# Optimization experiments

Measured on AMD Instinct MI355X. Metric: run time of the kernel, lower is better.

Reference implementation:

```python
import jax, jax.numpy as jnp
import numpy as np

NOISE_DIM = 100
HIDDEN = 256
VOCAB = 200
N_PHASES = 13
SEQ_LEN = 20
BATCH = 16384


def setup_inputs() -> dict:
    key = jax.random.key(0)
    ks = jax.random.split(key, 8)
    s = 0.05
    return {
        "noise": jax.random.normal(ks[0], (BATCH, NOISE_DIM), jnp.float32),
        "W_proj": jax.random.normal(ks[1], (HIDDEN, NOISE_DIM), jnp.float32) * s,
        "b_proj": jnp.zeros((HIDDEN,), jnp.float32),
        "W_ih": jax.random.normal(ks[2], (4 * HIDDEN, HIDDEN), jnp.float32) * s,
        "W_hh": jax.random.normal(ks[3], (4 * HIDDEN, HIDDEN), jnp.float32) * s,
        "b_ih": jnp.zeros((4 * HIDDEN,), jnp.float32),
        "b_hh": jnp.zeros((4 * HIDDEN,), jnp.float32),
        "W_tech": jax.random.normal(ks[4], (VOCAB, HIDDEN), jnp.float32) * s,
        "b_tech": jnp.zeros((VOCAB,), jnp.float32),
        "W_phase": jax.random.normal(ks[5], (N_PHASES, HIDDEN), jnp.float32) * s,
        "b_phase": jnp.zeros((N_PHASES,), jnp.float32),
        "W_time": jax.random.normal(ks[6], (1, HIDDEN), jnp.float32) * s,
        "b_time": jnp.zeros((1,), jnp.float32),
    }


def reference(noise, W_proj, b_proj, W_ih, W_hh, b_ih, b_hh,
              W_tech, b_tech, W_phase, b_phase, W_time, b_time):
    # initial_projection: x0 = Linear(noise)  -> first LSTM input
    x0 = noise @ W_proj.T + b_proj                      # [B, H]
    B = noise.shape[0]
    h0 = jnp.zeros((B, HIDDEN), noise.dtype)
    c0 = jnp.zeros((B, HIDDEN), noise.dtype)

    def step(carry, _):
        x, h, c = carry
        # torch LSTM gate order: i, f, g, o
        gates = x @ W_ih.T + b_ih + h @ W_hh.T + b_hh   # [B, 4H]
        i, f, g, o = jnp.split(gates, 4, axis=-1)
        i = jax.nn.sigmoid(i)
        f = jax.nn.sigmoid(f)
        g = jnp.tanh(g)
        o = jax.nn.sigmoid(o)
        c_new = f * c + i * g
        h_new = o * jnp.tanh(c_new)
        tech = h_new @ W_tech.T + b_tech                # [B, VOCAB]
        phase = h_new @ W_phase.T + b_phase             # [B, 13]
        timing = jax.nn.relu(h_new @ W_time.T + b_time) # [B, 1]
        out = jnp.concatenate([tech, phase, timing], axis=-1)  # [B, 214]
        # next step's LSTM input is the previous LSTM output (h_new)
        return (h_new, h_new, c_new), out

    _, outs = jax.lax.scan(step, (x0, h0, c0), None, length=SEQ_LEN)
    # outs: [SEQ_LEN, B, VOCAB + 13 + 1] = per-step [technique_logits | phase_logits | timing]
    return outs
```

## Files before the change

### kernel.cpp

```cpp
#include <hip/hip_runtime.h>
#include <stdint.h>

#define HID 256
#define BATCH 16384
#define SEQ 20
#define OUTF 214
#define BM 64
#define NBLK (BATCH/BM)
#define ROWE 264

typedef __attribute__((ext_vector_type(8))) short short8;
typedef __attribute__((ext_vector_type(4))) float f32x4;

#define MFMA(a,b,c) __builtin_amdgcn_mfma_f32_16x16x32_bf16((a),(b),(c),0,0,0)
#define SBAR() asm volatile("s_waitcnt lgkmcnt(0)\n\ts_barrier" ::: "memory")

__device__ __forceinline__ unsigned short f2bf(float f) {
    unsigned int u = __builtin_bit_cast(unsigned int, f);
    u += 0x7FFFu + ((u >> 16) & 1u);
    return (unsigned short)(u >> 16);
}
__device__ __forceinline__ float sigm(float x)     { return __fdividef(1.0f, 1.0f + __expf(-x)); }
__device__ __forceinline__ float tanhfast(float x) { return 1.0f - __fdividef(2.0f, __expf(2.0f*x) + 1.0f); }

__global__ __launch_bounds__(256) void prep_kernel(
    const float* __restrict__ W_proj, const float* __restrict__ W_ih,
    const float* __restrict__ W_hh,  const float* __restrict__ b_ih,
    const float* __restrict__ b_hh,  const float* __restrict__ W_tech,
    const float* __restrict__ b_tech, const float* __restrict__ W_phase,
    const float* __restrict__ b_phase, const float* __restrict__ W_time,
    const float* __restrict__ b_time,
    unsigned short* __restrict__ Wc, unsigned short* __restrict__ Wi,
    unsigned short* __restrict__ Wo, unsigned short* __restrict__ Wp,
    float* __restrict__ b_comb, float* __restrict__ b_out)
{
    const int n = blockIdx.x;
    const int k = threadIdx.x;
    const int lane = (n & 15) | (((k >> 3) & 3) << 4);
    const int e  = k & 7;
    const int tn = n >> 4;
    {
        float wi = W_ih[n*HID + k], wh = W_hh[n*HID + k];
        int idx = ((tn*8 + (k>>5))*64 + lane)*8 + e;
        Wi[idx] = f2bf(wi);
        Wc[idx] = f2bf(wi + wh);
    }
    if (n < 224) {
        float v = 0.0f;
        if (n < 200)       v = W_tech[n*HID + k];
        else if (n < 213)  v = W_phase[(n-200)*HID + k];
        else if (n == 213) v = W_time[k];
        int idx = ((tn*8 + (k>>5))*64 + lane)*8 + e;
        Wo[idx] = f2bf(v);
    }
    if (n < 256 && k < 128) {
        float v = (k < 100) ? W_proj[n*100 + k] : 0.0f;
        int idx = ((tn*4 + (k>>5))*64 + lane)*8 + e;
        Wp[idx] = f2bf(v);
    }
    if (n < 4) b_comb[n*256 + k] = b_ih[n*256 + k] + b_hh[n*256 + k];
    if (n == 4 && k < 224) {
        float v = 0.0f;
        if (k < 200)       v = b_tech[k];
        else if (k < 213)  v = b_phase[k-200];
        else if (k == 213) v = b_time[0];
        b_out[k] = v;
    }
}

__global__ __launch_bounds__(512, 2) void lstm_kernel(
    const float* __restrict__ noise, const float* __restrict__ b_proj,
    const unsigned short* __restrict__ Wc, const unsigned short* __restrict__ Wi,
    const unsigned short* __restrict__ Wo_g, const unsigned short* __restrict__ Wp,
    const float* __restrict__ b_comb, const float* __restrict__ b_out,
    float* __restrict__ out)
{
    __shared__ __attribute__((aligned(16))) unsigned short hbuf[2][BM * ROWE];
    __shared__ __attribute__((aligned(16))) float out_lds[BM * OUTF];

    const int tid  = threadIdx.x;
    const int w    = tid >> 6;
    const int lane = tid & 63;
    const int lr   = lane & 15;
    const int lq   = lane >> 4;
    const int blk  = blockIdx.x;

    {
        const float* nsrc = noise + (size_t)blk * BM * 100;
        for (int i = tid; i < BM*100; i += 512) {
            int m = i / 100; int kk = i - m*100;
            hbuf[1][m*ROWE + kk] = f2bf(nsrc[i]);
        }
        for (int i = tid; i < BM*28; i += 512) {
            int m = i / 28; int kk = i - m*28;
            hbuf[1][m*ROWE + 100 + kk] = 0;
        }
    }

    f32x4 bi[2][4];
    #pragma unroll
    for (int P = 0; P < 2; ++P)
        #pragma unroll
        for (int g = 0; g < 4; ++g)
            bi[P][g] = *(const f32x4*)&b_comb[g*256 + P*128 + w*16 + lq*4];
    f32x4 bo0 = *(const f32x4*)&b_out[w*16 + lq*4];
    f32x4 bo1 = {0.f,0.f,0.f,0.f};
    if (w < 6) bo1 = *(const f32x4*)&b_out[(8+w)*16 + lq*4];

    f32x4 c_[2][4];
    #pragma unroll
    for (int P = 0; P < 2; ++P)
        #pragma unroll
        for (int mt = 0; mt < 4; ++mt) c_[P][mt] = f32x4{0.f,0.f,0.f,0.f};

    SBAR();

    {
        f32x4 bp[2];
        #pragma unroll
        for (int jt = 0; jt < 2; ++jt)
            bp[jt] = *(const f32x4*)&b_proj[w*32 + jt*16 + lq*4];
        f32x4 acc[2][4];
        #pragma unroll
        for (int jt = 0; jt < 2; ++jt)
            #pragma unroll
            for (int mt = 0; mt < 4; ++mt) acc[jt][mt] = f32x4{0.f,0.f,0.f,0.f};
        #pragma unroll
        for (int kk = 0; kk < 4; ++kk) {
            short8 b[4];
            #pragma unroll
            for (int mt = 0; mt < 4; ++mt)
                b[mt] = *(const short8*)&hbuf[1][(mt*16+lr)*ROWE + kk*32 + lq*8];
            #pragma unroll
            for (int jt = 0; jt < 2; ++jt) {
                short8 a = *(const short8*)&Wp[(((w*2+jt)*4 + kk)*64 + lane)*8];
                #pragma unroll
                for (int mt = 0; mt < 4; ++mt)
                    acc[jt][mt] = MFMA(a, b[mt], acc[jt][mt]);
            }
        }
        #pragma unroll
        for (int jt = 0; jt < 2; ++jt) {
            const int jb = w*32 + jt*16 + lq*4;
            #pragma unroll
            for (int mt = 0; mt < 4; ++mt) {
                f32x4 v = acc[jt][mt] + bp[jt];
                unsigned int p0 = (unsigned int)f2bf(v.x) | ((unsigned int)f2bf(v.y) << 16);
                unsigned int p1 = (unsigned int)f2bf(v.z) | ((unsigned int)f2bf(v.w) << 16);
                uint2 pk; pk.x = p0; pk.y = p1;
                *(uint2*)&hbuf[0][(mt*16+lr)*ROWE + jb] = pk;
            }
        }
    }
    SBAR();

    auto gepass = [&](int P, const unsigned short* __restrict__ Wf, int pc) {
        f32x4 acc[4][4];
        #pragma unroll
        for (int g = 0; g < 4; ++g)
            #pragma unroll
            for (int mt = 0; mt < 4; ++mt) acc[g][mt] = f32x4{0.f,0.f,0.f,0.f};
        #pragma unroll
        for (int kk = 0; kk < 8; ++kk) {
            short8 b[4];
            #pragma unroll
            for (int mt = 0; mt < 4; ++mt)
                b[mt] = *(const short8*)&hbuf[pc][(mt*16+lr)*ROWE + kk*32 + lq*8];
            #pragma unroll
            for (int g = 0; g < 4; ++g) {
                short8 a = *(const short8*)&Wf[(((g*16 + P*8 + w)*8 + kk)*64 + lane)*8];
                #pragma unroll
                for (int mt = 0; mt < 4; ++mt)
                    acc[g][mt] = MFMA(a, b[mt], acc[g][mt]);
            }
        }
        const int jb = P*128 + w*16 + lq*4;
        #pragma unroll
        for (int mt = 0; mt < 4; ++mt) {
            f32x4 xi = acc[0][mt] + bi[P][0];
            f32x4 xf = acc[1][mt] + bi[P][1];
            f32x4 xg = acc[2][mt] + bi[P][2];
            f32x4 xo = acc[3][mt] + bi[P][3];
            f32x4 cc = c_[P][mt];
            float hh[4];
            #pragma unroll
            for (int r = 0; r < 4; ++r) {
                float iv = sigm(xi[r]);
                float fv = sigm(xf[r]);
                float gv = tanhfast(xg[r]);
                float ov = sigm(xo[r]);
                float cn = fv*cc[r] + iv*gv;
                cc[r] = cn;
                hh[r] = ov * tanhfast(cn);
            }
            c_[P][mt] = cc;
            unsigned int p0 = (unsigned int)f2bf(hh[0]) | ((unsigned int)f2bf(hh[1]) << 16);
            unsigned int p1 = (unsigned int)f2bf(hh[2]) | ((unsigned int)f2bf(hh[3]) << 16);
            uint2 pk; pk.x = p0; pk.y = p1;
            *(uint2*)&hbuf[pc^1][(mt*16+lr)*ROWE + jb] = pk;
        }
    };

    auto oproj = [&](int pc) {
        f32x4 oa0[4], oa1[4];
        #pragma unroll
        for (int mt = 0; mt < 4; ++mt) { oa0[mt] = f32x4{0.f,0.f,0.f,0.f}; oa1[mt] = f32x4{0.f,0.f,0.f,0.f}; }
        #pragma unroll
        for (int kk = 0; kk < 8; ++kk) {
            short8 b[4];
            #pragma unroll
            for (int mt = 0; mt < 4; ++mt)
                b[mt] = *(const short8*)&hbuf[pc][(mt*16+lr)*ROWE + kk*32 + lq*8];
            short8 a0 = *(const short8*)&Wo_g[((w*8 + kk)*64 + lane)*8];
            #pragma unroll
            for (int mt = 0; mt < 4; ++mt) oa0[mt] = MFMA(a0, b[mt], oa0[mt]);
            if (w < 6) {
                short8 a1 = *(const short8*)&Wo_g[(((8+w)*8 + kk)*64 + lane)*8];
                #pragma unroll
                for (int mt = 0; mt < 4; ++mt) oa1[mt] = MFMA(a1, b[mt], oa1[mt]);
            }
        }
        const int col0 = w*16 + lq*4;
        #pragma unroll
        for (int mt = 0; mt < 4; ++mt) {
            int row = mt*16 + lr;
            f32x4 v = oa0[mt] + bo0;
            float2 lo; lo.x = v.x; lo.y = v.y;
            float2 hi; hi.x = v.z; hi.y = v.w;
            *(float2*)&out_lds[row*OUTF + col0]     = lo;
            *(float2*)&out_lds[row*OUTF + col0 + 2] = hi;
        }
        if (w < 5) {
            const int col1 = 128 + w*16 + lq*4;
            #pragma unroll
            for (int mt = 0; mt < 4; ++mt) {
                int row = mt*16 + lr;
                f32x4 v = oa1[mt] + bo1;
                float2 lo; lo.x = v.x; lo.y = v.y;
                float2 hi; hi.x = v.z; hi.y = v.w;
                *(float2*)&out_lds[row*OUTF + col1]     = lo;
                *(float2*)&out_lds[row*OUTF + col1 + 2] = hi;
            }
        } else if (w == 5) {
            const int col1 = 208 + lq*4;
            #pragma unroll
            for (int mt = 0; mt < 4; ++mt) {
                int row = mt*16 + lr;
                f32x4 v = oa1[mt] + bo1;
                if (lq == 0) {
                    float2 lo; lo.x = v.x; lo.y = v.y;
                    float2 hi; hi.x = v.z; hi.y = v.w;
                    *(float2*)&out_lds[row*OUTF + col1]     = lo;
                    *(float2*)&out_lds[row*OUTF + col1 + 2] = hi;
                } else if (lq == 1) {
                    float2 lo; lo.x = v.x; lo.y = (v.y > 0.f) ? v.y : 0.f;
                    *(float2*)&out_lds[row*OUTF + col1] = lo;
                }
            }
        }
    };

    auto copy_out = [&](int t) {
        f32x4* dst = (f32x4*)(out + (size_t)t * BATCH * OUTF + (size_t)blk * BM * OUTF);
        const f32x4* src = (const f32x4*)out_lds;
        for (int i = tid; i < BM*OUTF/4; i += 512)
            __builtin_nontemporal_store(src[i], &dst[i]);
    };

    int p = 0;
    for (int t = 0; t < SEQ; ++t) {
        if (t > 0) copy_out(t-1);
        const unsigned short* Wf = t ? Wc : Wi;
        gepass(0, Wf, p);
        gepass(1, Wf, p);
        SBAR();
        oproj(p^1);
        p ^= 1;
        SBAR();
    }
    copy_out(SEQ-1);
}

extern "C" void kernel_launch(void* const* d_in, const int* in_sizes, int n_in,
                              void* d_out, int out_size, void* d_ws, size_t ws_size,
                              hipStream_t stream) {
    const float* noise   = (const float*)d_in[0];
    const float* W_proj  = (const float*)d_in[1];
    const float* b_proj  = (const float*)d_in[2];
    const float* W_ih    = (const float*)d_in[3];
    const float* W_hh    = (const float*)d_in[4];
    const float* b_ih    = (const float*)d_in[5];
    const float* b_hh    = (const float*)d_in[6];
    const float* W_tech  = (const float*)d_in[7];
    const float* b_tech  = (const float*)d_in[8];
    const float* W_phase = (const float*)d_in[9];
    const float* b_phase = (const float*)d_in[10];
    const float* W_time  = (const float*)d_in[11];
    const float* b_time  = (const float*)d_in[12];

    char* ws = (char*)d_ws;
    unsigned short* Wc = (unsigned short*)(ws);
    unsigned short* Wi = (unsigned short*)(ws + 524288);
    unsigned short* Wo = (unsigned short*)(ws + 1048576);
    unsigned short* Wp = (unsigned short*)(ws + 1163264);
    float* b_comb = (float*)(ws + 1228800);
    float* b_out  = (float*)(ws + 1232896);

    prep_kernel<<<1024, 256, 0, stream>>>(W_proj, W_ih, W_hh, b_ih, b_hh,
                                          W_tech, b_tech, W_phase, b_phase, W_time, b_time,
                                          Wc, Wi, Wo, Wp, b_comb, b_out);
    lstm_kernel<<<NBLK, 512, 0, stream>>>(noise, b_proj, Wc, Wi, Wo, Wp, b_comb, b_out,
                                          (float*)d_out);
}
```

Before: 470.3 us.

## Drop per-step barrier by skewing output projection and per-wave column copy-out

The output projection now runs one timestep later, at the start of the next iteration, reading the previous hidden buffer. Each wave copies out only the columns it wrote itself, two steps behind, so the second block-wide barrier per timestep is removed. The LDS staging rows are padded to 216 floats so fragments can be written as 16-byte vectors, and the wave index is made scalar with readfirstlane. In exchange, the global stores become 8-byte, row-per-lane writes with a large stride instead of the earlier linear 16-byte coalesced stream, which may hurt write efficiency.

```diff
diff --git a/kernel.cpp b/kernel.cpp
--- a/kernel.cpp
+++ b/kernel.cpp
@@ -8,9 +8,11 @@
 #define BM 64
 #define NBLK (BATCH/BM)
 #define ROWE 264
+#define OLD 216
 
 typedef __attribute__((ext_vector_type(8))) short short8;
 typedef __attribute__((ext_vector_type(4))) float f32x4;
+typedef __attribute__((ext_vector_type(2))) float f32x2;
 
 #define MFMA(a,b,c) __builtin_amdgcn_mfma_f32_16x16x32_bf16((a),(b),(c),0,0,0)
 #define SBAR() asm volatile("s_waitcnt lgkmcnt(0)\n\ts_barrier" ::: "memory")
@@ -76,10 +78,10 @@
     float* __restrict__ out)
 {
     __shared__ __attribute__((aligned(16))) unsigned short hbuf[2][BM * ROWE];
-    __shared__ __attribute__((aligned(16))) float out_lds[BM * OUTF];
+    __shared__ __attribute__((aligned(16))) float out_lds[BM * OLD];
 
     const int tid  = threadIdx.x;
-    const int w    = tid >> 6;
+    const int w    = __builtin_amdgcn_readfirstlane(tid) >> 6;
     const int lane = tid & 63;
     const int lr   = lane & 15;
     const int lq   = lane >> 4;
@@ -224,61 +226,93 @@
         #pragma unroll
         for (int mt = 0; mt < 4; ++mt) {
             int row = mt*16 + lr;
-            f32x4 v = oa0[mt] + bo0;
-            float2 lo; lo.x = v.x; lo.y = v.y;
-            float2 hi; hi.x = v.z; hi.y = v.w;
-            *(float2*)&out_lds[row*OUTF + col0]     = lo;
-            *(float2*)&out_lds[row*OUTF + col0 + 2] = hi;
+            *(f32x4*)&out_lds[row*OLD + col0] = oa0[mt] + bo0;
         }
         if (w < 5) {
             const int col1 = 128 + w*16 + lq*4;
             #pragma unroll
             for (int mt = 0; mt < 4; ++mt) {
                 int row = mt*16 + lr;
-                f32x4 v = oa1[mt] + bo1;
-                float2 lo; lo.x = v.x; lo.y = v.y;
-                float2 hi; hi.x = v.z; hi.y = v.w;
-                *(float2*)&out_lds[row*OUTF + col1]     = lo;
-                *(float2*)&out_lds[row*OUTF + col1 + 2] = hi;
+                *(f32x4*)&out_lds[row*OLD + col1] = oa1[mt] + bo1;
             }
         } else if (w == 5) {
-            const int col1 = 208 + lq*4;
             #pragma unroll
             for (int mt = 0; mt < 4; ++mt) {
                 int row = mt*16 + lr;
                 f32x4 v = oa1[mt] + bo1;
                 if (lq == 0) {
-                    float2 lo; lo.x = v.x; lo.y = v.y;
-                    float2 hi; hi.x = v.z; hi.y = v.w;
-                    *(float2*)&out_lds[row*OUTF + col1]     = lo;
-                    *(float2*)&out_lds[row*OUTF + col1 + 2] = hi;
+                    *(f32x4*)&out_lds[row*OLD + 208] = v;
                 } else if (lq == 1) {
-                    float2 lo; lo.x = v.x; lo.y = (v.y > 0.f) ? v.y : 0.f;
-                    *(float2*)&out_lds[row*OUTF + col1] = lo;
+                    f32x2 lo; lo.x = v.x; lo.y = (v.y > 0.f) ? v.y : 0.f;
+                    *(f32x2*)&out_lds[row*OLD + 212] = lo;
                 }
             }
         }
     };
 
-    auto copy_out = [&](int t) {
-        f32x4* dst = (f32x4*)(out + (size_t)t * BATCH * OUTF + (size_t)blk * BM * OUTF);
-        const f32x4* src = (const f32x4*)out_lds;
-        for (int i = tid; i < BM*OUTF/4; i += 512)
-            __builtin_nontemporal_store(src[i], &dst[i]);
+    auto copy_cols = [&](int t) {
+        float* outt = out + (size_t)t * BATCH * OUTF + (size_t)blk * BM * OUTF;
+        const int row = lane;
+        {
+            const int cb = w*16;
+            const float* src = &out_lds[row*OLD + cb];
+            float* dst = &outt[(size_t)row*OUTF + cb];
+            f32x4 v0 = *(const f32x4*)(src);
+            f32x4 v1 = *(const f32x4*)(src + 4);
+            f32x4 v2 = *(const f32x4*)(src + 8);
+            f32x4 v3 = *(const f32x4*)(src + 12);
+            f32x2 s;
+            s.x=v0.x; s.y=v0.y; __builtin_nontemporal_store(s, (f32x2*)(dst+0));
+            s.x=v0.z; s.y=v0.w; __builtin_nontemporal_store(s, (f32x2*)(dst+2));
+            s.x=v1.x; s.y=v1.y; __builtin_nontemporal_store(s, (f32x2*)(dst+4));
+            s.x=v1.z; s.y=v1.w; __builtin_nontemporal_store(s, (f32x2*)(dst+6));
+            s.x=v2.x; s.y=v2.y; __builtin_nontemporal_store(s, (f32x2*)(dst+8));
+            s.x=v2.z; s.y=v2.w; __builtin_nontemporal_store(s, (f32x2*)(dst+10));
+            s.x=v3.x; s.y=v3.y; __builtin_nontemporal_store(s, (f32x2*)(dst+12));
+            s.x=v3.z; s.y=v3.w; __builtin_nontemporal_store(s, (f32x2*)(dst+14));
+        }
+        if (w < 5) {
+            const int cb = 128 + w*16;
+            const float* src = &out_lds[row*OLD + cb];
+            float* dst = &outt[(size_t)row*OUTF + cb];
+            f32x4 v0 = *(const f32x4*)(src);
+            f32x4 v1 = *(const f32x4*)(src + 4);
+            f32x4 v2 = *(const f32x4*)(src + 8);
+            f32x4 v3 = *(const f32x4*)(src + 12);
+            f32x2 s;
+            s.x=v0.x; s.y=v0.y; __builtin_nontemporal_store(s, (f32x2*)(dst+0));
+            s.x=v0.z; s.y=v0.w; __builtin_nontemporal_store(s, (f32x2*)(dst+2));
+            s.x=v1.x; s.y=v1.y; __builtin_nontemporal_store(s, (f32x2*)(dst+4));
+            s.x=v1.z; s.y=v1.w; __builtin_nontemporal_store(s, (f32x2*)(dst+6));
+            s.x=v2.x; s.y=v2.y; __builtin_nontemporal_store(s, (f32x2*)(dst+8));
+            s.x=v2.z; s.y=v2.w; __builtin_nontemporal_store(s, (f32x2*)(dst+10));
+            s.x=v3.x; s.y=v3.y; __builtin_nontemporal_store(s, (f32x2*)(dst+12));
+            s.x=v3.z; s.y=v3.w; __builtin_nontemporal_store(s, (f32x2*)(dst+14));
+        } else if (w == 5) {
+            const float* src = &out_lds[row*OLD + 208];
+            float* dst = &outt[(size_t)row*OUTF + 208];
+            f32x4 v0 = *(const f32x4*)(src);
+            f32x2 v2 = *(const f32x2*)(src + 4);
+            f32x2 s;
+            s.x=v0.x; s.y=v0.y; __builtin_nontemporal_store(s, (f32x2*)(dst+0));
+            s.x=v0.z; s.y=v0.w; __builtin_nontemporal_store(s, (f32x2*)(dst+2));
+            __builtin_nontemporal_store(v2, (f32x2*)(dst+4));
+        }
     };
 
     int p = 0;
     for (int t = 0; t < SEQ; ++t) {
-        if (t > 0) copy_out(t-1);
+        if (t >= 2) copy_cols(t-2);
+        if (t >= 1) oproj(p);
         const unsigned short* Wf = t ? Wc : Wi;
         gepass(0, Wf, p);
         gepass(1, Wf, p);
         SBAR();
-        oproj(p^1);
         p ^= 1;
-        SBAR();
-    }
-    copy_out(SEQ-1);
+    }
+    copy_cols(SEQ-2);
+    oproj(p);
+    copy_cols(SEQ-1);
 }
 
 extern "C" void kernel_launch(void* const* d_in, const int* in_sizes, int n_in,
```

After: 1.237 ms. +163.0%, slower.

## Double block to 1024 threads, one wave per gate column slice

Applied to the files above, without the earlier changes.

Doubles the workgroup to 16 waves. Each wave now owns one 16-column slice of the hidden state for all four gates, so the two sequential gate passes per step become one. The output projection is spread over 14 waves, one tile each. Biases are staged in LDS instead of registers, and bf16 packing uses the hardware v_cvt_pk_bf16_f32 instruction. The aim is more parallelism and fewer registers per wave, at the cost of more waves synchronizing at each barrier and launch bounds that may force register limits or spilling.

```diff
diff --git a/kernel.cpp b/kernel.cpp
--- a/kernel.cpp
+++ b/kernel.cpp
@@ -11,6 +11,7 @@
 
 typedef __attribute__((ext_vector_type(8))) short short8;
 typedef __attribute__((ext_vector_type(4))) float f32x4;
+typedef __attribute__((ext_vector_type(2))) float f32x2;
 
 #define MFMA(a,b,c) __builtin_amdgcn_mfma_f32_16x16x32_bf16((a),(b),(c),0,0,0)
 #define SBAR() asm volatile("s_waitcnt lgkmcnt(0)\n\ts_barrier" ::: "memory")
@@ -19,6 +20,11 @@
     unsigned int u = __builtin_bit_cast(unsigned int, f);
     u += 0x7FFFu + ((u >> 16) & 1u);
     return (unsigned short)(u >> 16);
+}
+__device__ __forceinline__ unsigned int cvtpk(float lo, float hi) {
+    unsigned int r;
+    asm("v_cvt_pk_bf16_f32 %0, %1, %2" : "=v"(r) : "v"(lo), "v"(hi));
+    return r;
 }
 __device__ __forceinline__ float sigm(float x)     { return __fdividef(1.0f, 1.0f + __expf(-x)); }
 __device__ __forceinline__ float tanhfast(float x) { return 1.0f - __fdividef(2.0f, __expf(2.0f*x) + 1.0f); }
@@ -68,7 +74,7 @@
     }
 }
 
-__global__ __launch_bounds__(512, 2) void lstm_kernel(
+__global__ __launch_bounds__(1024, 4) void lstm_kernel(
     const float* __restrict__ noise, const float* __restrict__ b_proj,
     const unsigned short* __restrict__ Wc, const unsigned short* __restrict__ Wi,
     const unsigned short* __restrict__ Wo_g, const unsigned short* __restrict__ Wp,
@@ -77,9 +83,11 @@
 {
     __shared__ __attribute__((aligned(16))) unsigned short hbuf[2][BM * ROWE];
     __shared__ __attribute__((aligned(16))) float out_lds[BM * OUTF];
+    __shared__ __attribute__((aligned(16))) float bi_lds[1024];
+    __shared__ __attribute__((aligned(16))) float bo_lds[224];
 
     const int tid  = threadIdx.x;
-    const int w    = tid >> 6;
+    const int w    = __builtin_amdgcn_readfirstlane(tid) >> 6;
     const int lane = tid & 63;
     const int lr   = lane & 15;
     const int lq   = lane >> 4;
@@ -87,74 +95,51 @@
 
     {
         const float* nsrc = noise + (size_t)blk * BM * 100;
-        for (int i = tid; i < BM*100; i += 512) {
+        for (int i = tid; i < BM*100; i += 1024) {
             int m = i / 100; int kk = i - m*100;
             hbuf[1][m*ROWE + kk] = f2bf(nsrc[i]);
         }
-        for (int i = tid; i < BM*28; i += 512) {
+        for (int i = tid; i < BM*28; i += 1024) {
             int m = i / 28; int kk = i - m*28;
             hbuf[1][m*ROWE + 100 + kk] = 0;
         }
-    }
-
-    f32x4 bi[2][4];
+        bi_lds[tid] = b_comb[tid];
+        if (tid < 224) bo_lds[tid] = b_out[tid];
+    }
+
+    f32x4 c_[4];
     #pragma unroll
-    for (int P = 0; P < 2; ++P)
-        #pragma unroll
-        for (int g = 0; g < 4; ++g)
-            bi[P][g] = *(const f32x4*)&b_comb[g*256 + P*128 + w*16 + lq*4];
-    f32x4 bo0 = *(const f32x4*)&b_out[w*16 + lq*4];
-    f32x4 bo1 = {0.f,0.f,0.f,0.f};
-    if (w < 6) bo1 = *(const f32x4*)&b_out[(8+w)*16 + lq*4];
-
-    f32x4 c_[2][4];
-    #pragma unroll
-    for (int P = 0; P < 2; ++P)
-        #pragma unroll
-        for (int mt = 0; mt < 4; ++mt) c_[P][mt] = f32x4{0.f,0.f,0.f,0.f};
+    for (int mt = 0; mt < 4; ++mt) c_[mt] = f32x4{0.f,0.f,0.f,0.f};
 
     SBAR();
 
     {
-        f32x4 bp[2];
-        #pragma unroll
-        for (int jt = 0; jt < 2; ++jt)
-            bp[jt] = *(const f32x4*)&b_proj[w*32 + jt*16 + lq*4];
-        f32x4 acc[2][4];
-        #pragma unroll
-        for (int jt = 0; jt < 2; ++jt)
-            #pragma unroll
-            for (int mt = 0; mt < 4; ++mt) acc[jt][mt] = f32x4{0.f,0.f,0.f,0.f};
+        f32x4 acc[4];
+        #pragma unroll
+        for (int mt = 0; mt < 4; ++mt) acc[mt] = f32x4{0.f,0.f,0.f,0.f};
         #pragma unroll
         for (int kk = 0; kk < 4; ++kk) {
             short8 b[4];
             #pragma unroll
             for (int mt = 0; mt < 4; ++mt)
                 b[mt] = *(const short8*)&hbuf[1][(mt*16+lr)*ROWE + kk*32 + lq*8];
-            #pragma unroll
-            for (int jt = 0; jt < 2; ++jt) {
-                short8 a = *(const short8*)&Wp[(((w*2+jt)*4 + kk)*64 + lane)*8];
-                #pragma unroll
-                for (int mt = 0; mt < 4; ++mt)
-                    acc[jt][mt] = MFMA(a, b[mt], acc[jt][mt]);
-            }
-        }
-        #pragma unroll
-        for (int jt = 0; jt < 2; ++jt) {
-            const int jb = w*32 + jt*16 + lq*4;
-            #pragma unroll
-            for (int mt = 0; mt < 4; ++mt) {
-                f32x4 v = acc[jt][mt] + bp[jt];
-                unsigned int p0 = (unsigned int)f2bf(v.x) | ((unsigned int)f2bf(v.y) << 16);
-                unsigned int p1 = (unsigned int)f2bf(v.z) | ((unsigned int)f2bf(v.w) << 16);
-                uint2 pk; pk.x = p0; pk.y = p1;
-                *(uint2*)&hbuf[0][(mt*16+lr)*ROWE + jb] = pk;
-            }
+            short8 a = *(const short8*)&Wp[((w*4 + kk)*64 + lane)*8];
+            #pragma unroll
+            for (int mt = 0; mt < 4; ++mt)
+                acc[mt] = MFMA(a, b[mt], acc[mt]);
+        }
+        f32x4 bp = *(const f32x4*)&b_proj[w*16 + lq*4];
+        const int jb = w*16 + lq*4;
+        #pragma unroll
+        for (int mt = 0; mt < 4; ++mt) {
+            f32x4 v = acc[mt] + bp;
+            uint2 pk; pk.x = cvtpk(v.x, v.y); pk.y = cvtpk(v.z, v.w);
+            *(uint2*)&hbuf[0][(mt*16+lr)*ROWE + jb] = pk;
         }
     }
     SBAR();
 
-    auto gepass = [&](int P, const unsigned short* __restrict__ Wf, int pc) {
+    auto gepass = [&](const unsigned short* __restrict__ Wf, int pc) {
         f32x4 acc[4][4];
         #pragma unroll
         for (int g = 0; g < 4; ++g)
@@ -168,20 +153,24 @@
                 b[mt] = *(const short8*)&hbuf[pc][(mt*16+lr)*ROWE + kk*32 + lq*8];
             #pragma unroll
             for (int g = 0; g < 4; ++g) {
-                short8 a = *(const short8*)&Wf[(((g*16 + P*8 + w)*8 + kk)*64 + lane)*8];
+                short8 a = *(const short8*)&Wf[(((g*16 + w)*8 + kk)*64 + lane)*8];
                 #pragma unroll
                 for (int mt = 0; mt < 4; ++mt)
                     acc[g][mt] = MFMA(a, b[mt], acc[g][mt]);
             }
         }
-        const int jb = P*128 + w*16 + lq*4;
+        const int jb = w*16 + lq*4;
+        f32x4 bi0 = *(const f32x4*)&bi_lds[0*256 + jb];
+        f32x4 bi1 = *(const f32x4*)&bi_lds[1*256 + jb];
+        f32x4 bi2 = *(const f32x4*)&bi_lds[2*256 + jb];
+        f32x4 bi3 = *(const f32x4*)&bi_lds[3*256 + jb];
         #pragma unroll
         for (int mt = 0; mt < 4; ++mt) {
-            f32x4 xi = acc[0][mt] + bi[P][0];
-            f32x4 xf = acc[1][mt] + bi[P][1];
-            f32x4 xg = acc[2][mt] + bi[P][2];
-            f32x4 xo = acc[3][mt] + bi[P][3];
-            f32x4 cc = c_[P][mt];
+            f32x4 xi = acc[0][mt] + bi0;
+            f32x4 xf = acc[1][mt] + bi1;
+            f32x4 xg = acc[2][mt] + bi2;
+            f32x4 xo = acc[3][mt] + bi3;
+            f32x4 cc = c_[mt];
             float hh[4];
             #pragma unroll
             for (int r = 0; r < 4; ++r) {
@@ -193,92 +182,73 @@
                 cc[r] = cn;
                 hh[r] = ov * tanhfast(cn);
             }
-            c_[P][mt] = cc;
-            unsigned int p0 = (unsigned int)f2bf(hh[0]) | ((unsigned int)f2bf(hh[1]) << 16);
-            unsigned int p1 = (unsigned int)f2bf(hh[2]) | ((unsigned int)f2bf(hh[3]) << 16);
-            uint2 pk; pk.x = p0; pk.y = p1;
+            c_[mt] = cc;
+            uint2 pk; pk.x = cvtpk(hh[0], hh[1]); pk.y = cvtpk(hh[2], hh[3]);
             *(uint2*)&hbuf[pc^1][(mt*16+lr)*ROWE + jb] = pk;
         }
     };
 
     auto oproj = [&](int pc) {
-        f32x4 oa0[4], oa1[4];
-        #pragma unroll
-        for (int mt = 0; mt < 4; ++mt) { oa0[mt] = f32x4{0.f,0.f,0.f,0.f}; oa1[mt] = f32x4{0.f,0.f,0.f,0.f}; }
+        if (w >= 14) return;
+        f32x4 oa[4];
+        #pragma unroll
+        for (int mt = 0; mt < 4; ++mt) oa[mt] = f32x4{0.f,0.f,0.f,0.f};
         #pragma unroll
         for (int kk = 0; kk < 8; ++kk) {
             short8 b[4];
             #pragma unroll
             for (int mt = 0; mt < 4; ++mt)
                 b[mt] = *(const short8*)&hbuf[pc][(mt*16+lr)*ROWE + kk*32 + lq*8];
-            short8 a0 = *(const short8*)&Wo_g[((w*8 + kk)*64 + lane)*8];
-            #pragma unroll
-            for (int mt = 0; mt < 4; ++mt) oa0[mt] = MFMA(a0, b[mt], oa0[mt]);
-            if (w < 6) {
-                short8 a1 = *(const short8*)&Wo_g[(((8+w)*8 + kk)*64 + lane)*8];
-                #pragma unroll
-                for (int mt = 0; mt < 4; ++mt) oa1[mt] = MFMA(a1, b[mt], oa1[mt]);
-            }
-        }
-        const int col0 = w*16 + lq*4;
+            short8 a = *(const short8*)&Wo_g[((w*8 + kk)*64 + lane)*8];
+            #pragma unroll
+            for (int mt = 0; mt < 4; ++mt) oa[mt] = MFMA(a, b[mt], oa[mt]);
+        }
+        f32x4 bo = *(const f32x4*)&bo_lds[w*16 + lq*4];
+        const int col = w*16 + lq*4;
         #pragma unroll
         for (int mt = 0; mt < 4; ++mt) {
             int row = mt*16 + lr;
-            f32x4 v = oa0[mt] + bo0;
-            float2 lo; lo.x = v.x; lo.y = v.y;
-            float2 hi; hi.x = v.z; hi.y = v.w;
-            *(float2*)&out_lds[row*OUTF + col0]     = lo;
-            *(float2*)&out_lds[row*OUTF + col0 + 2] = hi;
-        }
-        if (w < 5) {
-            const int col1 = 128 + w*16 + lq*4;
-            #pragma unroll
-            for (int mt = 0; mt < 4; ++mt) {
-                int row = mt*16 + lr;
-                f32x4 v = oa1[mt] + bo1;
-                float2 lo; lo.x = v.x; lo.y = v.y;
-                float2 hi; hi.x = v.z; hi.y = v.w;
-                *(float2*)&out_lds[row*OUTF + col1]     = lo;
-                *(float2*)&out_lds[row*OUTF + col1 + 2] = hi;
-            }
-        } else if (w == 5) {
-            const int col1 = 208 + lq*4;
-            #pragma unroll
-            for (int mt = 0; mt < 4; ++mt) {
-                int row = mt*16 + lr;
-                f32x4 v = oa1[mt] + bo1;
+            f32x4 v = oa[mt] + bo;
+            if (w < 13) {
+                f32x2 lo; lo.x = v.x; lo.y = v.y;
+                f32x2 hi; hi.x = v.z; hi.y = v.w;
+                *(f32x2*)&out_lds[row*OUTF + col]     = lo;
+                *(f32x2*)&out_lds[row*OUTF + col + 2] = hi;
+            } else {
                 if (lq == 0) {
-                    float2 lo; lo.x = v.x; lo.y = v.y;
-                    float2 hi; hi.x = v.z; hi.y = v.w;
-                    *(float2*)&out_lds[row*OUTF + col1]     = lo;
-                    *(float2*)&out_lds[row*OUTF + col1 + 2] = hi;
+                    f32x2 lo; lo.x = v.x; lo.y = v.y;
+                    f32x2 hi; hi.x = v.z; hi.y = v.w;
+                    *(f32x2*)&out_lds[row*OUTF + 208] = lo;
+                    *(f32x2*)&out_lds[row*OUTF + 210] = hi;
                 } else if (lq == 1) {
-                    float2 lo; lo.x = v.x; lo.y = (v.y > 0.f) ? v.y : 0.f;
-                    *(float2*)&out_lds[row*OUTF + col1] = lo;
+                    f32x2 lo; lo.x = v.x; lo.y = (v.y > 0.f) ? v.y : 0.f;
+                    *(f32x2*)&out_lds[row*OUTF + 212] = lo;
                 }
             }
         }
     };
 
-    auto copy_out = [&](int t) {
+    auto copy_flat = [&](int t) {
         f32x4* dst = (f32x4*)(out + (size_t)t * BATCH * OUTF + (size_t)blk * BM * OUTF);
         const f32x4* src = (const f32x4*)out_lds;
-        for (int i = tid; i < BM*OUTF/4; i += 512)
-            __builtin_nontemporal_store(src[i], &dst[i]);
+        #pragma unroll
+        for (int it = 0; it < 4; ++it) {
+            int i = tid + it*1024;
+            if (i < BM*OUTF/4)
+                __builtin_nontemporal_store(src[i], &dst[i]);
+        }
     };
 
     int p = 0;
     for (int t = 0; t < SEQ; ++t) {
-        if (t > 0) copy_out(t-1);
-        const unsigned short* Wf = t ? Wc : Wi;
-        gepass(0, Wf, p);
-        gepass(1, Wf, p);
+        if (t > 0) copy_flat(t-1);
+        gepass(t ? Wc : Wi, p);
         SBAR();
         oproj(p^1);
         p ^= 1;
         SBAR();
     }
-    copy_out(SEQ-1);
+    copy_flat(SEQ-1);
 }
 
 extern "C" void kernel_launch(void* const* d_in, const int* in_sizes, int n_in,
@@ -309,6 +279,6 @@
     prep_kernel<<<1024, 256, 0, stream>>>(W_proj, W_ih, W_hh, b_ih, b_hh,
                                           W_tech, b_tech, W_phase, b_phase, W_time, b_time,
                                           Wc, Wi, Wo, Wp, b_comb, b_out);
-    lstm_kernel<<<NBLK, 512, 0, stream>>>(noise, b_proj, Wc, Wi, Wo, Wp, b_comb, b_out,
-                                          (float*)d_out);
-}
+    lstm_kernel<<<NBLK, 1024, 0, stream>>>(noise, b_proj, Wc, Wi, Wo, Wp, b_comb, b_out,
+                                           (float*)d_out);
+}
```

Measured after the change: 670.1 us. 1.42x slower.

## Fuse output projection of previous step into gate pass and use packed bf16 convert

Applied to the files above, without the earlier changes.

The output projection for step t-1 now runs inside the second gate pass of step t, reusing the same h tiles loaded from LDS, so one LDS read sweep per step is removed. The output copy is therefore deferred by two steps, and a final oproj-only pass is added after the loop. Biases move from registers into LDS to reduce register pressure, and manual bf16 rounding is replaced with the v_cvt_pk_bf16_f32 instruction. This adds more live accumulators in passB and changes the barrier layout.

```diff
diff --git a/kernel.cpp b/kernel.cpp
--- a/kernel.cpp
+++ b/kernel.cpp
@@ -11,6 +11,7 @@
 
 typedef __attribute__((ext_vector_type(8))) short short8;
 typedef __attribute__((ext_vector_type(4))) float f32x4;
+typedef __attribute__((ext_vector_type(2))) float f32x2;
 
 #define MFMA(a,b,c) __builtin_amdgcn_mfma_f32_16x16x32_bf16((a),(b),(c),0,0,0)
 #define SBAR() asm volatile("s_waitcnt lgkmcnt(0)\n\ts_barrier" ::: "memory")
@@ -19,6 +20,11 @@
     unsigned int u = __builtin_bit_cast(unsigned int, f);
     u += 0x7FFFu + ((u >> 16) & 1u);
     return (unsigned short)(u >> 16);
+}
+__device__ __forceinline__ unsigned int cvtpk(float lo, float hi) {
+    unsigned int r;
+    asm("v_cvt_pk_bf16_f32 %0, %1, %2" : "=v"(r) : "v"(lo), "v"(hi));
+    return r;
 }
 __device__ __forceinline__ float sigm(float x)     { return __fdividef(1.0f, 1.0f + __expf(-x)); }
 __device__ __forceinline__ float tanhfast(float x) { return 1.0f - __fdividef(2.0f, __expf(2.0f*x) + 1.0f); }
@@ -77,6 +83,8 @@
 {
     __shared__ __attribute__((aligned(16))) unsigned short hbuf[2][BM * ROWE];
     __shared__ __attribute__((aligned(16))) float out_lds[BM * OUTF];
+    __shared__ __attribute__((aligned(16))) float bi_lds[1024];
+    __shared__ __attribute__((aligned(16))) float bo_lds[224];
 
     const int tid  = threadIdx.x;
     const int w    = tid >> 6;
@@ -95,17 +103,10 @@
             int m = i / 28; int kk = i - m*28;
             hbuf[1][m*ROWE + 100 + kk] = 0;
         }
-    }
-
-    f32x4 bi[2][4];
-    #pragma unroll
-    for (int P = 0; P < 2; ++P)
-        #pragma unroll
-        for (int g = 0; g < 4; ++g)
-            bi[P][g] = *(const f32x4*)&b_comb[g*256 + P*128 + w*16 + lq*4];
-    f32x4 bo0 = *(const f32x4*)&b_out[w*16 + lq*4];
-    f32x4 bo1 = {0.f,0.f,0.f,0.f};
-    if (w < 6) bo1 = *(const f32x4*)&b_out[(8+w)*16 + lq*4];
+        bi_lds[tid] = b_comb[tid];
+        bi_lds[tid + 512] = b_comb[tid + 512];
+        if (tid < 224) bo_lds[tid] = b_out[tid];
+    }
 
     f32x4 c_[2][4];
     #pragma unroll
@@ -116,10 +117,6 @@
     SBAR();
 
     {
-        f32x4 bp[2];
-        #pragma unroll
-        for (int jt = 0; jt < 2; ++jt)
-            bp[jt] = *(const f32x4*)&b_proj[w*32 + jt*16 + lq*4];
         f32x4 acc[2][4];
         #pragma unroll
         for (int jt = 0; jt < 2; ++jt)
@@ -142,45 +139,28 @@
         #pragma unroll
         for (int jt = 0; jt < 2; ++jt) {
             const int jb = w*32 + jt*16 + lq*4;
+            f32x4 bp = *(const f32x4*)&b_proj[jb];
             #pragma unroll
             for (int mt = 0; mt < 4; ++mt) {
-                f32x4 v = acc[jt][mt] + bp[jt];
-                unsigned int p0 = (unsigned int)f2bf(v.x) | ((unsigned int)f2bf(v.y) << 16);
-                unsigned int p1 = (unsigned int)f2bf(v.z) | ((unsigned int)f2bf(v.w) << 16);
-                uint2 pk; pk.x = p0; pk.y = p1;
+                f32x4 v = acc[jt][mt] + bp;
+                uint2 pk; pk.x = cvtpk(v.x, v.y); pk.y = cvtpk(v.z, v.w);
                 *(uint2*)&hbuf[0][(mt*16+lr)*ROWE + jb] = pk;
             }
         }
     }
-    SBAR();
-
-    auto gepass = [&](int P, const unsigned short* __restrict__ Wf, int pc) {
-        f32x4 acc[4][4];
-        #pragma unroll
-        for (int g = 0; g < 4; ++g)
-            #pragma unroll
-            for (int mt = 0; mt < 4; ++mt) acc[g][mt] = f32x4{0.f,0.f,0.f,0.f};
-        #pragma unroll
-        for (int kk = 0; kk < 8; ++kk) {
-            short8 b[4];
-            #pragma unroll
-            for (int mt = 0; mt < 4; ++mt)
-                b[mt] = *(const short8*)&hbuf[pc][(mt*16+lr)*ROWE + kk*32 + lq*8];
-            #pragma unroll
-            for (int g = 0; g < 4; ++g) {
-                short8 a = *(const short8*)&Wf[(((g*16 + P*8 + w)*8 + kk)*64 + lane)*8];
-                #pragma unroll
-                for (int mt = 0; mt < 4; ++mt)
-                    acc[g][mt] = MFMA(a, b[mt], acc[g][mt]);
-            }
-        }
+
+    auto elemwise = [&](int P, f32x4 (&acc)[4][4], int pc) {
         const int jb = P*128 + w*16 + lq*4;
+        f32x4 bi0 = *(const f32x4*)&bi_lds[0*256 + jb];
+        f32x4 bi1 = *(const f32x4*)&bi_lds[1*256 + jb];
+        f32x4 bi2 = *(const f32x4*)&bi_lds[2*256 + jb];
+        f32x4 bi3 = *(const f32x4*)&bi_lds[3*256 + jb];
         #pragma unroll
         for (int mt = 0; mt < 4; ++mt) {
-            f32x4 xi = acc[0][mt] + bi[P][0];
-            f32x4 xf = acc[1][mt] + bi[P][1];
-            f32x4 xg = acc[2][mt] + bi[P][2];
-            f32x4 xo = acc[3][mt] + bi[P][3];
+            f32x4 xi = acc[0][mt] + bi0;
+            f32x4 xf = acc[1][mt] + bi1;
+            f32x4 xg = acc[2][mt] + bi2;
+            f32x4 xo = acc[3][mt] + bi3;
             f32x4 cc = c_[P][mt];
             float hh[4];
             #pragma unroll
@@ -194,14 +174,113 @@
                 hh[r] = ov * tanhfast(cn);
             }
             c_[P][mt] = cc;
-            unsigned int p0 = (unsigned int)f2bf(hh[0]) | ((unsigned int)f2bf(hh[1]) << 16);
-            unsigned int p1 = (unsigned int)f2bf(hh[2]) | ((unsigned int)f2bf(hh[3]) << 16);
-            uint2 pk; pk.x = p0; pk.y = p1;
+            uint2 pk; pk.x = cvtpk(hh[0], hh[1]); pk.y = cvtpk(hh[2], hh[3]);
             *(uint2*)&hbuf[pc^1][(mt*16+lr)*ROWE + jb] = pk;
         }
     };
 
-    auto oproj = [&](int pc) {
+    auto passA = [&](const unsigned short* __restrict__ Wf, int pc) {
+        f32x4 acc[4][4];
+        #pragma unroll
+        for (int g = 0; g < 4; ++g)
+            #pragma unroll
+            for (int mt = 0; mt < 4; ++mt) acc[g][mt] = f32x4{0.f,0.f,0.f,0.f};
+        #pragma unroll
+        for (int kk = 0; kk < 8; ++kk) {
+            short8 b[4];
+            #pragma unroll
+            for (int mt = 0; mt < 4; ++mt)
+                b[mt] = *(const short8*)&hbuf[pc][(mt*16+lr)*ROWE + kk*32 + lq*8];
+            #pragma unroll
+            for (int g = 0; g < 4; ++g) {
+                short8 a = *(const short8*)&Wf[(((g*16 + w)*8 + kk)*64 + lane)*8];
+                #pragma unroll
+                for (int mt = 0; mt < 4; ++mt)
+                    acc[g][mt] = MFMA(a, b[mt], acc[g][mt]);
+            }
+        }
+        elemwise(0, acc, pc);
+    };
+
+    auto passB = [&](const unsigned short* __restrict__ Wf, int pc, bool dowrite) {
+        f32x4 acc[4][4];
+        f32x4 oa0[4], oa1[4];
+        #pragma unroll
+        for (int g = 0; g < 4; ++g)
+            #pragma unroll
+            for (int mt = 0; mt < 4; ++mt) acc[g][mt] = f32x4{0.f,0.f,0.f,0.f};
+        #pragma unroll
+        for (int mt = 0; mt < 4; ++mt) { oa0[mt] = f32x4{0.f,0.f,0.f,0.f}; oa1[mt] = f32x4{0.f,0.f,0.f,0.f}; }
+        #pragma unroll
+        for (int kk = 0; kk < 8; ++kk) {
+            short8 b[4];
+            #pragma unroll
+            for (int mt = 0; mt < 4; ++mt)
+                b[mt] = *(const short8*)&hbuf[pc][(mt*16+lr)*ROWE + kk*32 + lq*8];
+            #pragma unroll
+            for (int g = 0; g < 4; ++g) {
+                short8 a = *(const short8*)&Wf[(((g*16 + 8 + w)*8 + kk)*64 + lane)*8];
+                #pragma unroll
+                for (int mt = 0; mt < 4; ++mt)
+                    acc[g][mt] = MFMA(a, b[mt], acc[g][mt]);
+            }
+            {
+                short8 a0 = *(const short8*)&Wo_g[((w*8 + kk)*64 + lane)*8];
+                #pragma unroll
+                for (int mt = 0; mt < 4; ++mt) oa0[mt] = MFMA(a0, b[mt], oa0[mt]);
+            }
+            if (w < 6) {
+                short8 a1 = *(const short8*)&Wo_g[(((8+w)*8 + kk)*64 + lane)*8];
+                #pragma unroll
+                for (int mt = 0; mt < 4; ++mt) oa1[mt] = MFMA(a1, b[mt], oa1[mt]);
+            }
+        }
+        elemwise(1, acc, pc);
+        if (dowrite) {
+            f32x4 bo0 = *(const f32x4*)&bo_lds[w*16 + lq*4];
+            const int col0 = w*16 + lq*4;
+            #pragma unroll
+            for (int mt = 0; mt < 4; ++mt) {
+                int row = mt*16 + lr;
+                f32x4 v = oa0[mt] + bo0;
+                f32x2 lo; lo.x = v.x; lo.y = v.y;
+                f32x2 hi; hi.x = v.z; hi.y = v.w;
+                *(f32x2*)&out_lds[row*OUTF + col0]     = lo;
+                *(f32x2*)&out_lds[row*OUTF + col0 + 2] = hi;
+            }
+            if (w < 5) {
+                f32x4 bo1 = *(const f32x4*)&bo_lds[(8+w)*16 + lq*4];
+                const int col1 = 128 + w*16 + lq*4;
+                #pragma unroll
+                for (int mt = 0; mt < 4; ++mt) {
+                    int row = mt*16 + lr;
+                    f32x4 v = oa1[mt] + bo1;
+                    f32x2 lo; lo.x = v.x; lo.y = v.y;
+                    f32x2 hi; hi.x = v.z; hi.y = v.w;
+                    *(f32x2*)&out_lds[row*OUTF + col1]     = lo;
+                    *(f32x2*)&out_lds[row*OUTF + col1 + 2] = hi;
+                }
+            } else if (w == 5) {
+                f32x4 bo1 = *(const f32x4*)&bo_lds[13*16 + lq*4];
+                #pragma unroll
+                for (int mt = 0; mt < 4; ++mt) {
+                    int row = mt*16 + lr;
+                    f32x4 v = oa1[mt] + bo1;
+                    if (lq == 0) {
+                        f32x2 lo; lo.x = v.x; lo.y = v.y;
+                        f32x2 hi; hi.x = v.z; hi.y = v.w;
+                        *(f32x2*)&out_lds[row*OUTF + 208] = lo;
+                        *(f32x2*)&out_lds[row*OUTF + 210] = hi;
+                    } else if (lq == 1) {
+                        f32x2 lo; lo.x = v.x; lo.y = (v.y > 0.f) ? v.y : 0.f;
+                        *(f32x2*)&out_lds[row*OUTF + 212] = lo;
+                    }
+                }
+            }
+        }
+    };
+
+    auto oproj_only = [&](int pc) {
         f32x4 oa0[4], oa1[4];
         #pragma unroll
         for (int mt = 0; mt < 4; ++mt) { oa0[mt] = f32x4{0.f,0.f,0.f,0.f}; oa1[mt] = f32x4{0.f,0.f,0.f,0.f}; }
@@ -220,47 +299,49 @@
                 for (int mt = 0; mt < 4; ++mt) oa1[mt] = MFMA(a1, b[mt], oa1[mt]);
             }
         }
+        f32x4 bo0 = *(const f32x4*)&bo_lds[w*16 + lq*4];
         const int col0 = w*16 + lq*4;
         #pragma unroll
         for (int mt = 0; mt < 4; ++mt) {
             int row = mt*16 + lr;
             f32x4 v = oa0[mt] + bo0;
-            float2 lo; lo.x = v.x; lo.y = v.y;
-            float2 hi; hi.x = v.z; hi.y = v.w;
-            *(float2*)&out_lds[row*OUTF + col0]     = lo;
-            *(float2*)&out_lds[row*OUTF + col0 + 2] = hi;
+            f32x2 lo; lo.x = v.x; lo.y = v.y;
+            f32x2 hi; hi.x = v.z; hi.y = v.w;
+            *(f32x2*)&out_lds[row*OUTF + col0]     = lo;
+            *(f32x2*)&out_lds[row*OUTF + col0 + 2] = hi;
         }
         if (w < 5) {
+            f32x4 bo1 = *(const f32x4*)&bo_lds[(8+w)*16 + lq*4];
             const int col1 = 128 + w*16 + lq*4;
             #pragma unroll
             for (int mt = 0; mt < 4; ++mt) {
                 int row = mt*16 + lr;
                 f32x4 v = oa1[mt] + bo1;
-                float2 lo; lo.x = v.x; lo.y = v.y;
-                float2 hi; hi.x = v.z; hi.y = v.w;
-                *(float2*)&out_lds[row*OUTF + col1]     = lo;
-                *(float2*)&out_lds[row*OUTF + col1 + 2] = hi;
+                f32x2 lo; lo.x = v.x; lo.y = v.y;
+                f32x2 hi; hi.x = v.z; hi.y = v.w;
+                *(f32x2*)&out_lds[row*OUTF + col1]     = lo;
+                *(f32x2*)&out_lds[row*OUTF + col1 + 2] = hi;
             }
         } else if (w == 5) {
-            const int col1 = 208 + lq*4;
+            f32x4 bo1 = *(const f32x4*)&bo_lds[13*16 + lq*4];
             #pragma unroll
             for (int mt = 0; mt < 4; ++mt) {
                 int row = mt*16 + lr;
                 f32x4 v = oa1[mt] + bo1;
                 if (lq == 0) {
-                    float2 lo; lo.x = v.x; lo.y = v.y;
-                    float2 hi; hi.x = v.z; hi.y = v.w;
-                    *(float2*)&out_lds[row*OUTF + col1]     = lo;
-                    *(float2*)&out_lds[row*OUTF + col1 + 2] = hi;
+                    f32x2 lo; lo.x = v.x; lo.y = v.y;
+                    f32x2 hi; hi.x = v.z; hi.y = v.w;
+                    *(f32x2*)&out_lds[row*OUTF + 208] = lo;
+                    *(f32x2*)&out_lds[row*OUTF + 210] = hi;
                 } else if (lq == 1) {
-                    float2 lo; lo.x = v.x; lo.y = (v.y > 0.f) ? v.y : 0.f;
-                    *(float2*)&out_lds[row*OUTF + col1] = lo;
+                    f32x2 lo; lo.x = v.x; lo.y = (v.y > 0.f) ? v.y : 0.f;
+                    *(f32x2*)&out_lds[row*OUTF + 212] = lo;
                 }
             }
         }
     };
 
-    auto copy_out = [&](int t) {
+    auto copy_flat = [&](int t) {
         f32x4* dst = (f32x4*)(out + (size_t)t * BATCH * OUTF + (size_t)blk * BM * OUTF);
         const f32x4* src = (const f32x4*)out_lds;
         for (int i = tid; i < BM*OUTF/4; i += 512)
@@ -269,16 +350,19 @@
 
     int p = 0;
     for (int t = 0; t < SEQ; ++t) {
-        if (t > 0) copy_out(t-1);
+        if (t >= 2) copy_flat(t-2);
+        SBAR();
         const unsigned short* Wf = t ? Wc : Wi;
-        gepass(0, Wf, p);
-        gepass(1, Wf, p);
-        SBAR();
-        oproj(p^1);
+        passA(Wf, p);
+        passB(Wf, p, t > 0);
         p ^= 1;
         SBAR();
     }
-    copy_out(SEQ-1);
+    copy_flat(SEQ-2);
+    SBAR();
+    oproj_only(p);
+    SBAR();
+    copy_flat(SEQ-1);
 }
 
 extern "C" void kernel_launch(void* const* d_in, const int* in_sizes, int n_in,
```

Result: faster. 383.0 us (median of 2 runs) (-18.6%).
